# Kernel tuning notes

Hardware: AMD Instinct MI355X
Metric: run time of the kernel (lower is better)

## Reference

```python
import jax, jax.numpy as jnp
import numpy as np

B, H, L, TAU, THETA = 8192, 256, 4, 8, 8


def setup_inputs() -> dict:
    key = jax.random.key(0)
    ks = jax.random.split(key, 16)
    w = lambda k, shape: (jax.random.normal(k, shape, jnp.float32) * 0.02)
    return {
        "x": jax.random.normal(ks[0], (B, H), jnp.float32),
        "t_att": jax.random.normal(ks[1], (L, TAU, B, H), jnp.float32),
        "s_att": jax.random.normal(ks[2], (L, TAU, B, H), jnp.float32),
        "embed_w": w(ks[3], (H, H)),
        "embed_b": jnp.zeros((H,), jnp.float32),
        "wtn": w(ks[4], (L, H, H)),
        "btn": jnp.zeros((L, H), jnp.float32),
        "wsn": w(ks[5], (L, H, H)),
        "bsn": jnp.zeros((L, H), jnp.float32),
        "wt": w(ks[6], (L, 3 * H, H)),
        "bt": jnp.zeros((L, 3 * H), jnp.float32),
        "ws": w(ks[7], (L, 3 * H, H)),
        "bs": jnp.zeros((L, 3 * H), jnp.float32),
        "out_w": w(ks[8], (H, H)),
        "out_b": jnp.zeros((H,), jnp.float32),
    }


def _forward(x, t_att, s_att, embed_w, embed_b, wtn, btn, wsn, bsn, wt, bt, ws, bs, out_w, out_b):
    n_layers, tau = t_att.shape[0], t_att.shape[1]
    b, h = x.shape
    scale = 1.0 / np.sqrt(h).astype(np.float32)
    theta = THETA

    S = x @ embed_w.T + embed_b  # embed: [B, H]
    # rolling spatial buffers, start as theta zero entries
    t_sp = jnp.zeros((theta, b, h), x.dtype)
    s_sp = jnp.zeros((theta, b, h), x.dtype)

    for i in range(n_layers):
        T_last = t_att[i, -1]  # [B, H]
        # append current S_t / last T_t to spatial buffers, keep last theta
        s_sp = jnp.concatenate([s_sp[1:], S[None]], axis=0)
        t_sp = jnp.concatenate([t_sp[1:], T_last[None]], axis=0)
        # s_att[i].append(S_t); slice last tau -> keys include current S
        s_keys = jnp.concatenate([s_att[i, 1:], S[None]], axis=0)  # [tau, B, H]
        t_vals = t_att[i]  # [tau, B, H]

        s_next = S @ wsn[i].T + bsn[i]
        t_next = T_last @ wtn[i].T + btn[i]

        # temporal attention over last-tau history
        w_t = jax.nn.softmax(jnp.einsum('kbh,bh->kb', s_keys, s_next) * scale, axis=0)
        T_trend = jnp.einsum('kb,kbh->bh', w_t, t_vals)
        t_gate = jax.nn.sigmoid(t_next)
        T_fusion = T_last * t_gate + (1.0 - t_gate) * T_trend

        # spatial attention over last-theta buffer
        w_s = jax.nn.softmax(jnp.einsum('kbh,bh->kb', t_sp, t_next) * scale, axis=0)
        S_trend = jnp.einsum('kb,kbh->bh', w_s, s_sp)
        s_gate = jax.nn.sigmoid(s_next)
        S_fusion = S * s_gate + (1.0 - s_gate) * S_trend

        Tc = T_fusion @ wt[i].T + bt[i]  # [B, 3H]
        Sc = S_fusion @ ws[i].T + bs[i]
        t_g, t_t_, t_s_ = jnp.split(Tc, 3, axis=-1)
        s_g, s_t_, s_s_ = jnp.split(Sc, 3, axis=-1)
        Tg = jax.nn.sigmoid(t_g)
        Sg = jax.nn.sigmoid(s_g)
        # T_new feeds the (stateful) history; S carries to next layer
        S = Sg * s_s_ + (1.0 - Sg) * t_s_

    return jnp.tanh(S @ out_w.T + out_b)


def reference(x, t_att, s_att, embed_w, embed_b, wtn, btn, wsn, bsn, wt, bt, ws, bs, out_w, out_b):
    return _forward(x, t_att, s_att, embed_w, embed_b, wtn, btn, wsn, bsn, wt, bt, ws, bs, out_w, out_b)
```

## Files before the change

kernel.cpp:

```cpp
#include <hip/hip_runtime.h>
#include <cmath>

typedef __attribute__((ext_vector_type(8))) short short8;
typedef __attribute__((ext_vector_type(4))) float f32x4;
typedef __attribute__((ext_vector_type(4))) unsigned short us4;
typedef unsigned short u16;

#define BATCH 8192
#define HDIM  256
static constexpr size_t BH = (size_t)BATCH * HDIM;
#define LPAD 264

__device__ __forceinline__ u16 f2bf(float f) {
    union { float f; unsigned u; } v; v.f = f;
    unsigned r = v.u + 0x7FFFu + ((v.u >> 16) & 1u);
    return (u16)(r >> 16);
}
__device__ __forceinline__ float bf2f(u16 u) {
    union { unsigned u; float f; } v; v.u = ((unsigned)u) << 16;
    return v.f;
}
__device__ __forceinline__ float sigmoidf_(float x) {
    return 1.f / (1.f + __expf(-x));
}
__device__ __forceinline__ short8 cvt8(const float* p) {
    f32x4 lo = *(const f32x4*)p, hi = *(const f32x4*)(p + 4);
    short8 t;
    t[0] = (short)f2bf(lo[0]); t[1] = (short)f2bf(lo[1]);
    t[2] = (short)f2bf(lo[2]); t[3] = (short)f2bf(lo[3]);
    t[4] = (short)f2bf(hi[0]); t[5] = (short)f2bf(hi[1]);
    t[6] = (short)f2bf(hi[2]); t[7] = (short)f2bf(hi[3]);
    return t;
}
__device__ __forceinline__ float dot4(const f32x4& a, const float* b) {
    return a[0] * b[0] + a[1] * b[1] + a[2] * b[2] + a[3] * b[3];
}
template<int N>
__device__ __forceinline__ void vmwait() {
    asm volatile("s_waitcnt vmcnt(%0)" :: "n"(N) : "memory");
    __builtin_amdgcn_sched_barrier(0);
}

__global__ __launch_bounds__(256) void convert_weights(
    const float* __restrict__ embed_w, const float* __restrict__ wtn,
    const float* __restrict__ wsn, const float* __restrict__ wt,
    const float* __restrict__ ws, const float* __restrict__ out_w,
    u16* __restrict__ dst)
{
    int idx = blockIdx.x * 256 + threadIdx.x;
    int e = idx * 4;
    if (e >= 22 * 65536) return;
    int c = e >> 16, o = e & 65535;
    const float* src;
    if (c == 0)      src = embed_w + o;
    else if (c < 5)  src = wtn + (size_t)(c - 1) * 65536 + o;
    else if (c < 9)  src = wsn + (size_t)(c - 5) * 65536 + o;
    else if (c < 13) src = wt + (size_t)(c - 9) * 768 * 256 + 512 * 256 + o;
    else if (c < 17) src = ws + (size_t)(c - 13) * 768 * 256 + o;
    else if (c < 21) src = ws + (size_t)(c - 17) * 768 * 256 + 512 * 256 + o;
    else             src = out_w + o;
    f32x4 v = *(const f32x4*)src;
    us4 r;
#pragma unroll
    for (int j = 0; j < 4; ++j) r[j] = f2bf(v[j]);
    *(us4*)(dst + e) = r;
}

template<int I>
__device__ __forceinline__ void attn_row(
    const float* __restrict__ t_att, const float* __restrict__ s_att,
    const u16* __restrict__ S_hist,
    int brow, int rr, int lane,
    u16 (&sn_lds)[16][LPAD], u16 (&tn_lds)[16][LPAD],
    u16 (&tf_lds)[16][LPAD], u16 (&sf_lds)[16][LPAD])
{
    const float scale = 0.0625f;
    const size_t ro = (size_t)brow * 256 + lane * 4;
    const float* sa = s_att + (size_t)I * 8 * BH + ro;
    const float* ta = t_att + (size_t)I * 8 * BH + ro;

    us4 scu;
    us4 shu[I > 0 ? I : 1];
    asm volatile("global_load_dwordx2 %0, %1, off"
                 : "=v"(scu) : "v"(S_hist + (size_t)I * BH + ro));
#pragma unroll
    for (int jj = 0; jj < I; ++jj)
        asm volatile("global_load_dwordx2 %0, %1, off"
                     : "=v"(shu[jj]) : "v"(S_hist + (size_t)jj * BH + ro));

    f32x4 dbuf[8 + I];
#pragma unroll
    for (int kk = 0; kk < 7; ++kk)
        asm volatile("global_load_dwordx4 %0, %1, off"
                     : "=v"(dbuf[kk]) : "v"(sa + (size_t)(kk + 1) * BH));
#pragma unroll
    for (int jj = 0; jj < I; ++jj)
        asm volatile("global_load_dwordx4 %0, %1, off"
                     : "=v"(dbuf[7 + jj]) : "v"(t_att + ((size_t)jj * 8 + 7) * BH + ro));
    asm volatile("global_load_dwordx4 %0, %1, off"
                 : "=v"(dbuf[7 + I]) : "v"(ta + (size_t)7 * BH));

    f32x4 tbuf[7];
#pragma unroll
    for (int kk = 0; kk < 7; ++kk)
        asm volatile("global_load_dwordx4 %0, %1, off"
                     : "=v"(tbuf[kk]) : "v"(ta + (size_t)kk * BH));

    us4 snu = *(const us4*)&sn_lds[rr][lane * 4];
    us4 tnu = *(const us4*)&tn_lds[rr][lane * 4];
    float sn[4], tn[4];
#pragma unroll
    for (int j = 0; j < 4; ++j) { sn[j] = bf2f(snu[j]); tn[j] = bf2f(tnu[j]); }

    vmwait<7>();

    float Sc[4];
#pragma unroll
    for (int j = 0; j < 4; ++j) Sc[j] = bf2f(scu[j]);

    constexpr int NV = 9 + I;
    float v[NV];
#pragma unroll
    for (int kk = 0; kk < 7; ++kk) v[kk] = dot4(dbuf[kk], sn);
    v[7] = Sc[0] * sn[0] + Sc[1] * sn[1] + Sc[2] * sn[2] + Sc[3] * sn[3];
#pragma unroll
    for (int jj = 0; jj < I; ++jj) v[8 + jj] = dot4(dbuf[7 + jj], tn);
    v[8 + I] = dot4(dbuf[7 + I], tn);

#pragma unroll
    for (int o = 32; o > 0; o >>= 1)
#pragma unroll
        for (int u = 0; u < NV; ++u) v[u] += __shfl_xor(v[u], o);

    float m = v[0] * scale;
#pragma unroll
    for (int kk = 1; kk < 8; ++kk) m = fmaxf(m, v[kk] * scale);
    float w8[8], den = 0.f;
#pragma unroll
    for (int kk = 0; kk < 8; ++kk) { w8[kk] = __expf(v[kk] * scale - m); den += w8[kk]; }
    float inv = 1.f / den;

    vmwait<0>();

    float Tt[4];
#pragma unroll
    for (int j = 0; j < 4; ++j) Tt[j] = w8[7] * dbuf[7 + I][j];
#pragma unroll
    for (int kk = 0; kk < 7; ++kk)
#pragma unroll
        for (int j = 0; j < 4; ++j) Tt[j] += w8[kk] * tbuf[kk][j];
    us4 ot;
#pragma unroll
    for (int j = 0; j < 4; ++j) {
        float g = sigmoidf_(tn[j]);
        ot[j] = f2bf(dbuf[7 + I][j] * g + (1.f - g) * Tt[j] * inv);
    }
    *(us4*)&tf_lds[rr][lane * 4] = ot;

    float ms = fmaxf(0.f, v[8 + I] * scale);
#pragma unroll
    for (int jj = 0; jj < I; ++jj) ms = fmaxf(ms, v[8 + jj] * scale);
    float dens = (float)(7 - I) * __expf(-ms);
    float St[4];
    {
        float w = __expf(v[8 + I] * scale - ms);
        dens += w;
#pragma unroll
        for (int j = 0; j < 4; ++j) St[j] = w * Sc[j];
    }
#pragma unroll
    for (int jj = 0; jj < I; ++jj) {
        float w = __expf(v[8 + jj] * scale - ms);
        dens += w;
#pragma unroll
        for (int j = 0; j < 4; ++j) St[j] += w * bf2f(shu[jj][j]);
    }
    float invs = 1.f / dens;
    us4 os;
#pragma unroll
    for (int j = 0; j < 4; ++j) {
        float g = sigmoidf_(sn[j]);
        os[j] = f2bf(Sc[j] * g + (1.f - g) * St[j] * invs);
    }
    *(us4*)&sf_lds[rr][lane * 4] = os;
}

template<int I>
__device__ __forceinline__ void layer_body(
    const float* __restrict__ t_att, const float* __restrict__ s_att,
    u16* __restrict__ S_hist, const u16* __restrict__ Wbf,
    const float* __restrict__ btn, const float* __restrict__ bsn,
    const float* __restrict__ bt, const float* __restrict__ bs,
    u16 (&sn_lds)[16][LPAD], u16 (&tn_lds)[16][LPAD],
    u16 (&tf_lds)[16][LPAD], u16 (&sf_lds)[16][LPAD],
    int lane, int wave, int lr, int kg, int row0)
{
    {
        const int g = wave >> 1;
        const int n0 = (wave & 1) * 128;
        const u16* Wm = Wbf + (size_t)((g ? 1 : 5) + I) * 65536;
        const float* bias = (g ? btn : bsn) + I * 256;
        f32x4 acc[8] = {};
        for (int k0 = 0; k0 < 256; k0 += 32) {
            int k = k0 + kg * 8;
            short8 a;
            if (g == 0) a = *(const short8*)(S_hist + (size_t)I * BH + (size_t)(row0 + lr) * 256 + k);
            else        a = cvt8(t_att + ((size_t)I * 8 + 7) * BH + (size_t)(row0 + lr) * 256 + k);
#pragma unroll
            for (int nf = 0; nf < 8; ++nf) {
                short8 b = *(const short8*)(Wm + (size_t)(n0 + nf * 16 + lr) * 256 + k);
                acc[nf] = __builtin_amdgcn_mfma_f32_16x16x32_bf16(a, b, acc[nf], 0, 0, 0);
            }
        }
        u16 (*dst)[LPAD] = g ? tn_lds : sn_lds;
#pragma unroll
        for (int nf = 0; nf < 8; ++nf) {
            int n = n0 + nf * 16 + lr;
            float bn = bias[n];
#pragma unroll
            for (int r = 0; r < 4; ++r)
                dst[kg * 4 + r][n] = f2bf(acc[nf][r] + bn);
        }
    }
    __syncthreads();

#pragma unroll 1
    for (int q = 0; q < 4; ++q) {
        int rr = wave * 4 + q;
        attn_row<I>(t_att, s_att, S_hist, row0 + rr, rr, lane,
                    sn_lds, tn_lds, tf_lds, sf_lds);
    }
    __syncthreads();

    {
        const int n0 = wave * 64;
        const u16* Wt3 = Wbf + (size_t)(9  + I) * 65536;
        const u16* Ws1 = Wbf + (size_t)(13 + I) * 65536;
        const u16* Ws3 = Wbf + (size_t)(17 + I) * 65536;
        f32x4 aT[4] = {}, aG[4] = {}, aS[4] = {};
        for (int k0 = 0; k0 < 256; k0 += 32) {
            int k = k0 + kg * 8;
            short8 at = *(const short8*)(&tf_lds[lr][k]);
            short8 as = *(const short8*)(&sf_lds[lr][k]);
#pragma unroll
            for (int nf = 0; nf < 4; ++nf) {
                size_t wo = (size_t)(n0 + nf * 16 + lr) * 256 + k;
                aT[nf] = __builtin_amdgcn_mfma_f32_16x16x32_bf16(at, *(const short8*)(Wt3 + wo), aT[nf], 0, 0, 0);
                aG[nf] = __builtin_amdgcn_mfma_f32_16x16x32_bf16(as, *(const short8*)(Ws1 + wo), aG[nf], 0, 0, 0);
                aS[nf] = __builtin_amdgcn_mfma_f32_16x16x32_bf16(as, *(const short8*)(Ws3 + wo), aS[nf], 0, 0, 0);
            }
        }
        u16* Sout = S_hist + (size_t)(I + 1) * BH;
        const float* b1 = bt + I * 768 + 512;
        const float* b2 = bs + I * 768;
        const float* b3 = bs + I * 768 + 512;
#pragma unroll
        for (int nf = 0; nf < 4; ++nf) {
            int n = n0 + nf * 16 + lr;
            float bb1 = b1[n], bb2 = b2[n], bb3 = b3[n];
#pragma unroll
            for (int r = 0; r < 4; ++r) {
                float gv = sigmoidf_(aG[nf][r] + bb2);
                float vv = gv * (aS[nf][r] + bb3) + (1.f - gv) * (aT[nf][r] + bb1);
                Sout[(size_t)(row0 + kg * 4 + r) * 256 + n] = f2bf(vv);
            }
        }
    }
    __syncthreads();
}

__global__ __launch_bounds__(256, 2) void stau_mega(
    const float* __restrict__ x,
    const float* __restrict__ t_att, const float* __restrict__ s_att,
    u16* __restrict__ S_hist, const u16* __restrict__ Wbf,
    const float* __restrict__ embed_b,
    const float* __restrict__ btn, const float* __restrict__ bsn,
    const float* __restrict__ bt, const float* __restrict__ bs,
    const float* __restrict__ out_b,
    float* __restrict__ outp)
{
    __shared__ __align__(16) u16 sn_lds[16][LPAD];
    __shared__ __align__(16) u16 tn_lds[16][LPAD];
    __shared__ __align__(16) u16 tf_lds[16][LPAD];
    __shared__ __align__(16) u16 sf_lds[16][LPAD];

    const int lane = threadIdx.x & 63;
    const int wave = threadIdx.x >> 6;
    const int lr = lane & 15;
    const int kg = lane >> 4;
    const int row0 = blockIdx.x * 16;

    {
        const int n0 = wave * 64;
        f32x4 acc[4] = {};
        for (int k0 = 0; k0 < 256; k0 += 32) {
            int k = k0 + kg * 8;
            short8 a = cvt8(x + (size_t)(row0 + lr) * 256 + k);
#pragma unroll
            for (int nf = 0; nf < 4; ++nf) {
                short8 b = *(const short8*)(Wbf + (size_t)(n0 + nf * 16 + lr) * 256 + k);
                acc[nf] = __builtin_amdgcn_mfma_f32_16x16x32_bf16(a, b, acc[nf], 0, 0, 0);
            }
        }
#pragma unroll
        for (int nf = 0; nf < 4; ++nf) {
            int n = n0 + nf * 16 + lr;
            float bn = embed_b[n];
#pragma unroll
            for (int r = 0; r < 4; ++r)
                S_hist[(size_t)(row0 + kg * 4 + r) * 256 + n] = f2bf(acc[nf][r] + bn);
        }
    }
    __syncthreads();

    layer_body<0>(t_att, s_att, S_hist, Wbf, btn, bsn, bt, bs,
                  sn_lds, tn_lds, tf_lds, sf_lds, lane, wave, lr, kg, row0);
    layer_body<1>(t_att, s_att, S_hist, Wbf, btn, bsn, bt, bs,
                  sn_lds, tn_lds, tf_lds, sf_lds, lane, wave, lr, kg, row0);
    layer_body<2>(t_att, s_att, S_hist, Wbf, btn, bsn, bt, bs,
                  sn_lds, tn_lds, tf_lds, sf_lds, lane, wave, lr, kg, row0);
    layer_body<3>(t_att, s_att, S_hist, Wbf, btn, bsn, bt, bs,
                  sn_lds, tn_lds, tf_lds, sf_lds, lane, wave, lr, kg, row0);

    {
        const int n0 = wave * 64;
        const u16* Wo = Wbf + (size_t)21 * 65536;
        const u16* S4 = S_hist + (size_t)4 * BH;
        f32x4 acc[4] = {};
        for (int k0 = 0; k0 < 256; k0 += 32) {
            int k = k0 + kg * 8;
            short8 a = *(const short8*)(S4 + (size_t)(row0 + lr) * 256 + k);
#pragma unroll
            for (int nf = 0; nf < 4; ++nf) {
                short8 b = *(const short8*)(Wo + (size_t)(n0 + nf * 16 + lr) * 256 + k);
                acc[nf] = __builtin_amdgcn_mfma_f32_16x16x32_bf16(a, b, acc[nf], 0, 0, 0);
            }
        }
#pragma unroll
        for (int nf = 0; nf < 4; ++nf) {
            int n = n0 + nf * 16 + lr;
            float bn = out_b[n];
#pragma unroll
            for (int r = 0; r < 4; ++r)
                outp[(size_t)(row0 + kg * 4 + r) * 256 + n] = tanhf(acc[nf][r] + bn);
        }
    }
}

extern "C" void kernel_launch(void* const* d_in, const int* in_sizes, int n_in,
                              void* d_out, int out_size, void* d_ws, size_t ws_size,
                              hipStream_t stream)
{
    (void)in_sizes; (void)n_in; (void)out_size; (void)ws_size;
    const float* x       = (const float*)d_in[0];
    const float* t_att   = (const float*)d_in[1];
    const float* s_att   = (const float*)d_in[2];
    const float* embed_w = (const float*)d_in[3];
    const float* embed_b = (const float*)d_in[4];
    const float* wtn     = (const float*)d_in[5];
    const float* btn     = (const float*)d_in[6];
    const float* wsn     = (const float*)d_in[7];
    const float* bsn     = (const float*)d_in[8];
    const float* wt      = (const float*)d_in[9];
    const float* bt      = (const float*)d_in[10];
    const float* ws_in   = (const float*)d_in[11];
    const float* bs      = (const float*)d_in[12];
    const float* out_w   = (const float*)d_in[13];
    const float* out_b   = (const float*)d_in[14];

    u16* wsp    = (u16*)d_ws;
    u16* Wbf    = wsp;
    u16* S_hist = wsp + (size_t)22 * 65536;

    convert_weights<<<1408, 256, 0, stream>>>(embed_w, wtn, wsn, wt, ws_in, out_w, Wbf);

    stau_mega<<<BATCH / 16, 256, 0, stream>>>(
        x, t_att, s_att, S_hist, Wbf, embed_b, btn, bsn, bt, bs, out_b, (float*)d_out);
}
```

Measured before the change: 312.8 us.

## Warp-specialize mega kernel with async global-to-LDS staging of attention history

Restructures the fused kernel into 512-thread blocks of 4 rows, with 4 producer waves and 4 consumer waves. Producer waves stream the per-layer t_att/s_att history straight into double-buffered LDS slabs using global_load_lds, prefetching two layers ahead, and also compute the attention rows. Consumer waves run the MFMA projections. Each block now uses only 4 of the 16 MFMA rows, so most matrix work is padding. Weight reads per row also rise fourfold, and the large LDS footprint limits occupancy, in exchange for hiding the HBM latency of the history tensors.

Result: slower. 881.7 us (+181.9%).

```diff
diff --git a/kernel.cpp b/kernel.cpp
--- a/kernel.cpp
+++ b/kernel.cpp
@@ -1,5 +1,6 @@
 #include <hip/hip_runtime.h>
 #include <cmath>
+#include <type_traits>
 
 typedef __attribute__((ext_vector_type(8))) short short8;
 typedef __attribute__((ext_vector_type(4))) float f32x4;
@@ -7,9 +8,7 @@
 typedef unsigned short u16;
 
 #define BATCH 8192
-#define HDIM  256
-static constexpr size_t BH = (size_t)BATCH * HDIM;
-#define LPAD 264
+static constexpr size_t BH = (size_t)BATCH * 256;
 
 __device__ __forceinline__ u16 f2bf(float f) {
     union { float f; unsigned u; } v; v.f = f;
@@ -39,6 +38,18 @@
 __device__ __forceinline__ void vmwait() {
     asm volatile("s_waitcnt vmcnt(%0)" :: "n"(N) : "memory");
     __builtin_amdgcn_sched_barrier(0);
+}
+__device__ __forceinline__ void lgkm0() {
+    asm volatile("s_waitcnt lgkmcnt(0)" ::: "memory");
+    __builtin_amdgcn_sched_barrier(0);
+}
+__device__ __forceinline__ void bar() { __builtin_amdgcn_s_barrier(); }
+
+__device__ __forceinline__ void gl_lds16(const float* g, float* l) {
+    __builtin_amdgcn_global_load_lds(
+        (const __attribute__((address_space(1))) unsigned int*)(const void*)g,
+        (__attribute__((address_space(3))) unsigned int*)(void*)l,
+        16, 0, 0);
 }
 
 __global__ __launch_bounds__(256) void convert_weights(
@@ -66,66 +77,60 @@
     *(us4*)(dst + e) = r;
 }
 
+template<int J>
+__device__ __forceinline__ void stage_row(float* buf,
+    const float* __restrict__ t_att, const float* __restrict__ s_att,
+    int row0, int r, int lane)
+{
+    constexpr int NS = (J & 1) ? 18 : 17;
+    const size_t ro = (size_t)(row0 + r) * 256 + lane * 4;
+    float* base = buf + (size_t)r * NS * 256;
+#pragma unroll
+    for (int kk = 0; kk < 7; ++kk)
+        gl_lds16(s_att + ((size_t)J * 8 + 1 + kk) * BH + ro, base + kk * 256);
+#pragma unroll
+    for (int kk = 0; kk < 8; ++kk)
+        gl_lds16(t_att + ((size_t)J * 8 + kk) * BH + ro, base + (7 + kk) * 256);
+#pragma unroll
+    for (int jj = 0; jj < J; ++jj)
+        gl_lds16(t_att + ((size_t)jj * 8 + 7) * BH + ro, base + (15 + jj) * 256);
+}
+
+struct LState {
+    float slabA[4][17][256];
+    float slabB[4][18][256];
+    u16 snl[4][264];
+    u16 tnl[4][264];
+    u16 tfl[4][264];
+    u16 sfl[4][264];
+    u16 scsh[4][4][256];
+};
+
 template<int I>
-__device__ __forceinline__ void attn_row(
-    const float* __restrict__ t_att, const float* __restrict__ s_att,
-    const u16* __restrict__ S_hist,
-    int brow, int rr, int lane,
-    u16 (&sn_lds)[16][LPAD], u16 (&tn_lds)[16][LPAD],
-    u16 (&tf_lds)[16][LPAD], u16 (&sf_lds)[16][LPAD])
-{
+__device__ __forceinline__ void attn_row_lds(const float* cur, int r, int lane, LState& L)
+{
+    constexpr int NS = (I & 1) ? 18 : 17;
     const float scale = 0.0625f;
-    const size_t ro = (size_t)brow * 256 + lane * 4;
-    const float* sa = s_att + (size_t)I * 8 * BH + ro;
-    const float* ta = t_att + (size_t)I * 8 * BH + ro;
-
-    us4 scu;
-    us4 shu[I > 0 ? I : 1];
-    asm volatile("global_load_dwordx2 %0, %1, off"
-                 : "=v"(scu) : "v"(S_hist + (size_t)I * BH + ro));
-#pragma unroll
-    for (int jj = 0; jj < I; ++jj)
-        asm volatile("global_load_dwordx2 %0, %1, off"
-                     : "=v"(shu[jj]) : "v"(S_hist + (size_t)jj * BH + ro));
-
-    f32x4 dbuf[8 + I];
-#pragma unroll
-    for (int kk = 0; kk < 7; ++kk)
-        asm volatile("global_load_dwordx4 %0, %1, off"
-                     : "=v"(dbuf[kk]) : "v"(sa + (size_t)(kk + 1) * BH));
-#pragma unroll
-    for (int jj = 0; jj < I; ++jj)
-        asm volatile("global_load_dwordx4 %0, %1, off"
-                     : "=v"(dbuf[7 + jj]) : "v"(t_att + ((size_t)jj * 8 + 7) * BH + ro));
-    asm volatile("global_load_dwordx4 %0, %1, off"
-                 : "=v"(dbuf[7 + I]) : "v"(ta + (size_t)7 * BH));
-
-    f32x4 tbuf[7];
-#pragma unroll
-    for (int kk = 0; kk < 7; ++kk)
-        asm volatile("global_load_dwordx4 %0, %1, off"
-                     : "=v"(tbuf[kk]) : "v"(ta + (size_t)kk * BH));
-
-    us4 snu = *(const us4*)&sn_lds[rr][lane * 4];
-    us4 tnu = *(const us4*)&tn_lds[rr][lane * 4];
-    float sn[4], tn[4];
-#pragma unroll
-    for (int j = 0; j < 4; ++j) { sn[j] = bf2f(snu[j]); tn[j] = bf2f(tnu[j]); }
-
-    vmwait<7>();
-
-    float Sc[4];
-#pragma unroll
-    for (int j = 0; j < 4; ++j) Sc[j] = bf2f(scu[j]);
+    const float* rowp = cur + (size_t)r * NS * 256;
+
+    us4 snu = *(const us4*)&L.snl[r][lane * 4];
+    us4 tnu = *(const us4*)&L.tnl[r][lane * 4];
+    us4 scu = *(const us4*)&L.scsh[r][0][lane * 4];
+    float sn[4], tn[4], Sc[4];
+#pragma unroll
+    for (int j = 0; j < 4; ++j) { sn[j] = bf2f(snu[j]); tn[j] = bf2f(tnu[j]); Sc[j] = bf2f(scu[j]); }
 
     constexpr int NV = 9 + I;
     float v[NV];
 #pragma unroll
-    for (int kk = 0; kk < 7; ++kk) v[kk] = dot4(dbuf[kk], sn);
+    for (int kk = 0; kk < 7; ++kk)
+        v[kk] = dot4(*(const f32x4*)(rowp + kk * 256 + lane * 4), sn);
     v[7] = Sc[0] * sn[0] + Sc[1] * sn[1] + Sc[2] * sn[2] + Sc[3] * sn[3];
 #pragma unroll
-    for (int jj = 0; jj < I; ++jj) v[8 + jj] = dot4(dbuf[7 + jj], tn);
-    v[8 + I] = dot4(dbuf[7 + I], tn);
+    for (int jj = 0; jj < I; ++jj)
+        v[8 + jj] = dot4(*(const f32x4*)(rowp + (15 + jj) * 256 + lane * 4), tn);
+    f32x4 tav7 = *(const f32x4*)(rowp + 14 * 256 + lane * 4);
+    v[8 + I] = dot4(tav7, tn);
 
 #pragma unroll
     for (int o = 32; o > 0; o >>= 1)
@@ -140,22 +145,20 @@
     for (int kk = 0; kk < 8; ++kk) { w8[kk] = __expf(v[kk] * scale - m); den += w8[kk]; }
     float inv = 1.f / den;
 
-    vmwait<0>();
-
-    float Tt[4];
-#pragma unroll
-    for (int j = 0; j < 4; ++j) Tt[j] = w8[7] * dbuf[7 + I][j];
-#pragma unroll
-    for (int kk = 0; kk < 7; ++kk)
-#pragma unroll
-        for (int j = 0; j < 4; ++j) Tt[j] += w8[kk] * tbuf[kk][j];
+    float Tt[4] = {0.f, 0.f, 0.f, 0.f};
+#pragma unroll
+    for (int kk = 0; kk < 8; ++kk) {
+        f32x4 tv = *(const f32x4*)(rowp + (7 + kk) * 256 + lane * 4);
+#pragma unroll
+        for (int j = 0; j < 4; ++j) Tt[j] += w8[kk] * tv[j];
+    }
     us4 ot;
 #pragma unroll
     for (int j = 0; j < 4; ++j) {
         float g = sigmoidf_(tn[j]);
-        ot[j] = f2bf(dbuf[7 + I][j] * g + (1.f - g) * Tt[j] * inv);
-    }
-    *(us4*)&tf_lds[rr][lane * 4] = ot;
+        ot[j] = f2bf(tav7[j] * g + (1.f - g) * Tt[j] * inv);
+    }
+    *(us4*)&L.tfl[r][lane * 4] = ot;
 
     float ms = fmaxf(0.f, v[8 + I] * scale);
 #pragma unroll
@@ -172,8 +175,9 @@
     for (int jj = 0; jj < I; ++jj) {
         float w = __expf(v[8 + jj] * scale - ms);
         dens += w;
-#pragma unroll
-        for (int j = 0; j < 4; ++j) St[j] += w * bf2f(shu[jj][j]);
+        us4 shu = *(const us4*)&L.scsh[r][1 + jj][lane * 4];
+#pragma unroll
+        for (int j = 0; j < 4; ++j) St[j] += w * bf2f(shu[j]);
     }
     float invs = 1.f / dens;
     us4 os;
@@ -182,7 +186,7 @@
         float g = sigmoidf_(sn[j]);
         os[j] = f2bf(Sc[j] * g + (1.f - g) * St[j] * invs);
     }
-    *(us4*)&sf_lds[rr][lane * 4] = os;
+    *(us4*)&L.sfl[r][lane * 4] = os;
 }
 
 template<int I>
@@ -191,57 +195,69 @@
     u16* __restrict__ S_hist, const u16* __restrict__ Wbf,
     const float* __restrict__ btn, const float* __restrict__ bsn,
     const float* __restrict__ bt, const float* __restrict__ bs,
-    u16 (&sn_lds)[16][LPAD], u16 (&tn_lds)[16][LPAD],
-    u16 (&tf_lds)[16][LPAD], u16 (&sf_lds)[16][LPAD],
-    int lane, int wave, int lr, int kg, int row0)
-{
-    {
-        const int g = wave >> 1;
-        const int n0 = (wave & 1) * 128;
-        const u16* Wm = Wbf + (size_t)((g ? 1 : 5) + I) * 65536;
-        const float* bias = (g ? btn : bsn) + I * 256;
-        f32x4 acc[8] = {};
+    LState& L, int lane, int wave, int lr, int kg, int row0, bool prod, int pr, int n0)
+{
+    constexpr int NS = (I & 1) ? 18 : 17;
+    float* cur = (I & 1) ? &L.slabB[0][0][0] : &L.slabA[0][0][0];
+
+    if (!prod) {
+        const int cw = wave;
+        const size_t ro = (size_t)(row0 + cw) * 256 + lane * 4;
+        *(us4*)&L.scsh[cw][0][lane * 4] = *(const us4*)(S_hist + (size_t)I * BH + ro);
+#pragma unroll
+        for (int jj = 0; jj < I; ++jj)
+            *(us4*)&L.scsh[cw][1 + jj][lane * 4] = *(const us4*)(S_hist + (size_t)jj * BH + ro);
+
+        const u16* Wsn = Wbf + (size_t)(5 + I) * 65536;
+        const u16* Wtn = Wbf + (size_t)(1 + I) * 65536;
+        const u16* Arow = S_hist + (size_t)I * BH + (size_t)(row0 + (lr < 4 ? lr : 0)) * 256;
+        const float* Trow = cur + (size_t)(lr < 4 ? lr : 0) * NS * 256 + 14 * 256;
+        f32x4 accS[4] = {}, accT[4] = {};
         for (int k0 = 0; k0 < 256; k0 += 32) {
             int k = k0 + kg * 8;
-            short8 a;
-            if (g == 0) a = *(const short8*)(S_hist + (size_t)I * BH + (size_t)(row0 + lr) * 256 + k);
-            else        a = cvt8(t_att + ((size_t)I * 8 + 7) * BH + (size_t)(row0 + lr) * 256 + k);
-#pragma unroll
-            for (int nf = 0; nf < 8; ++nf) {
-                short8 b = *(const short8*)(Wm + (size_t)(n0 + nf * 16 + lr) * 256 + k);
-                acc[nf] = __builtin_amdgcn_mfma_f32_16x16x32_bf16(a, b, acc[nf], 0, 0, 0);
-            }
-        }
-        u16 (*dst)[LPAD] = g ? tn_lds : sn_lds;
-#pragma unroll
-        for (int nf = 0; nf < 8; ++nf) {
-            int n = n0 + nf * 16 + lr;
-            float bn = bias[n];
-#pragma unroll
-            for (int r = 0; r < 4; ++r)
-                dst[kg * 4 + r][n] = f2bf(acc[nf][r] + bn);
-        }
-    }
-    __syncthreads();
-
-#pragma unroll 1
-    for (int q = 0; q < 4; ++q) {
-        int rr = wave * 4 + q;
-        attn_row<I>(t_att, s_att, S_hist, row0 + rr, rr, lane,
-                    sn_lds, tn_lds, tf_lds, sf_lds);
-    }
-    __syncthreads();
-
-    {
-        const int n0 = wave * 64;
-        const u16* Wt3 = Wbf + (size_t)(9  + I) * 65536;
+            short8 aS = *(const short8*)(Arow + k);
+            short8 aT = cvt8(Trow + k);
+#pragma unroll
+            for (int nf = 0; nf < 4; ++nf) {
+                size_t wo = (size_t)(n0 + nf * 16 + lr) * 256 + k;
+                accS[nf] = __builtin_amdgcn_mfma_f32_16x16x32_bf16(aS, *(const short8*)(Wsn + wo), accS[nf], 0, 0, 0);
+                accT[nf] = __builtin_amdgcn_mfma_f32_16x16x32_bf16(aT, *(const short8*)(Wtn + wo), accT[nf], 0, 0, 0);
+            }
+        }
+        if (kg == 0) {
+#pragma unroll
+            for (int nf = 0; nf < 4; ++nf) {
+                int n = n0 + nf * 16 + lr;
+                float bS = bsn[I * 256 + n], bT = btn[I * 256 + n];
+#pragma unroll
+                for (int r = 0; r < 4; ++r) {
+                    L.snl[r][n] = f2bf(accS[nf][r] + bS);
+                    L.tnl[r][n] = f2bf(accT[nf][r] + bT);
+                }
+            }
+        }
+        lgkm0();
+    }
+    bar();
+
+    if (prod) {
+        attn_row_lds<I>(cur, pr, lane, L);
+        lgkm0();
+        if constexpr (I + 2 <= 3)
+            stage_row<I + 2>(cur, t_att, s_att, row0, pr, lane);
+    }
+    bar();
+
+    if (!prod) {
+        const u16* Wt3 = Wbf + (size_t)(9 + I) * 65536;
         const u16* Ws1 = Wbf + (size_t)(13 + I) * 65536;
         const u16* Ws3 = Wbf + (size_t)(17 + I) * 65536;
+        const int ar = (lr < 4 ? lr : 0);
         f32x4 aT[4] = {}, aG[4] = {}, aS[4] = {};
         for (int k0 = 0; k0 < 256; k0 += 32) {
             int k = k0 + kg * 8;
-            short8 at = *(const short8*)(&tf_lds[lr][k]);
-            short8 as = *(const short8*)(&sf_lds[lr][k]);
+            short8 at = *(const short8*)(&L.tfl[ar][k]);
+            short8 as = *(const short8*)(&L.sfl[ar][k]);
 #pragma unroll
             for (int nf = 0; nf < 4; ++nf) {
                 size_t wo = (size_t)(n0 + nf * 16 + lr) * 256 + k;
@@ -250,26 +266,32 @@
                 aS[nf] = __builtin_amdgcn_mfma_f32_16x16x32_bf16(as, *(const short8*)(Ws3 + wo), aS[nf], 0, 0, 0);
             }
         }
-        u16* Sout = S_hist + (size_t)(I + 1) * BH;
-        const float* b1 = bt + I * 768 + 512;
-        const float* b2 = bs + I * 768;
-        const float* b3 = bs + I * 768 + 512;
-#pragma unroll
-        for (int nf = 0; nf < 4; ++nf) {
-            int n = n0 + nf * 16 + lr;
-            float bb1 = b1[n], bb2 = b2[n], bb3 = b3[n];
-#pragma unroll
-            for (int r = 0; r < 4; ++r) {
-                float gv = sigmoidf_(aG[nf][r] + bb2);
-                float vv = gv * (aS[nf][r] + bb3) + (1.f - gv) * (aT[nf][r] + bb1);
-                Sout[(size_t)(row0 + kg * 4 + r) * 256 + n] = f2bf(vv);
-            }
-        }
-    }
-    __syncthreads();
-}
-
-__global__ __launch_bounds__(256, 2) void stau_mega(
+        if (kg == 0) {
+            const float* b1 = bt + I * 768 + 512;
+            const float* b2 = bs + I * 768;
+            const float* b3 = bs + I * 768 + 512;
+#pragma unroll
+            for (int nf = 0; nf < 4; ++nf) {
+                int n = n0 + nf * 16 + lr;
+                float bb1 = b1[n], bb2 = b2[n], bb3 = b3[n];
+#pragma unroll
+                for (int r = 0; r < 4; ++r) {
+                    float gv = sigmoidf_(aG[nf][r] + bb2);
+                    float vv = gv * (aS[nf][r] + bb3) + (1.f - gv) * (aT[nf][r] + bb1);
+                    S_hist[(size_t)(I + 1) * BH + (size_t)(row0 + r) * 256 + n] = f2bf(vv);
+                }
+            }
+        }
+        vmwait<0>();
+    } else {
+        if constexpr (I == 0) vmwait<17>();
+        else if constexpr (I == 1) vmwait<18>();
+        else if constexpr (I == 2) vmwait<0>();
+    }
+    bar();
+}
+
+__global__ __launch_bounds__(512, 2) void stau_mega(
     const float* __restrict__ x,
     const float* __restrict__ t_att, const float* __restrict__ s_att,
     u16* __restrict__ S_hist, const u16* __restrict__ Wbf,
@@ -279,70 +301,74 @@
     const float* __restrict__ out_b,
     float* __restrict__ outp)
 {
-    __shared__ __align__(16) u16 sn_lds[16][LPAD];
-    __shared__ __align__(16) u16 tn_lds[16][LPAD];
-    __shared__ __align__(16) u16 tf_lds[16][LPAD];
-    __shared__ __align__(16) u16 sf_lds[16][LPAD];
+    __shared__ __align__(16) LState L;
 
     const int lane = threadIdx.x & 63;
     const int wave = threadIdx.x >> 6;
     const int lr = lane & 15;
     const int kg = lane >> 4;
-    const int row0 = blockIdx.x * 16;
-
-    {
-        const int n0 = wave * 64;
+    const int row0 = blockIdx.x * 4;
+    const bool prod = wave >= 4;
+    const int pr = wave - 4;
+    const int n0 = (wave & 3) * 64;
+
+    if (prod) {
+        stage_row<0>(&L.slabA[0][0][0], t_att, s_att, row0, pr, lane);
+        stage_row<1>(&L.slabB[0][0][0], t_att, s_att, row0, pr, lane);
+        vmwait<16>();
+    } else {
+        const float* Ax = x + (size_t)(row0 + (lr < 4 ? lr : 0)) * 256;
         f32x4 acc[4] = {};
         for (int k0 = 0; k0 < 256; k0 += 32) {
             int k = k0 + kg * 8;
-            short8 a = cvt8(x + (size_t)(row0 + lr) * 256 + k);
+            short8 a = cvt8(Ax + k);
 #pragma unroll
             for (int nf = 0; nf < 4; ++nf) {
                 short8 b = *(const short8*)(Wbf + (size_t)(n0 + nf * 16 + lr) * 256 + k);
                 acc[nf] = __builtin_amdgcn_mfma_f32_16x16x32_bf16(a, b, acc[nf], 0, 0, 0);
             }
         }
-#pragma unroll
-        for (int nf = 0; nf < 4; ++nf) {
-            int n = n0 + nf * 16 + lr;
-            float bn = embed_b[n];
-#pragma unroll
-            for (int r = 0; r < 4; ++r)
-                S_hist[(size_t)(row0 + kg * 4 + r) * 256 + n] = f2bf(acc[nf][r] + bn);
-        }
-    }
-    __syncthreads();
-
-    layer_body<0>(t_att, s_att, S_hist, Wbf, btn, bsn, bt, bs,
-                  sn_lds, tn_lds, tf_lds, sf_lds, lane, wave, lr, kg, row0);
-    layer_body<1>(t_att, s_att, S_hist, Wbf, btn, bsn, bt, bs,
-                  sn_lds, tn_lds, tf_lds, sf_lds, lane, wave, lr, kg, row0);
-    layer_body<2>(t_att, s_att, S_hist, Wbf, btn, bsn, bt, bs,
-                  sn_lds, tn_lds, tf_lds, sf_lds, lane, wave, lr, kg, row0);
-    layer_body<3>(t_att, s_att, S_hist, Wbf, btn, bsn, bt, bs,
-                  sn_lds, tn_lds, tf_lds, sf_lds, lane, wave, lr, kg, row0);
-
-    {
-        const int n0 = wave * 64;
+        if (kg == 0) {
+#pragma unroll
+            for (int nf = 0; nf < 4; ++nf) {
+                int n = n0 + nf * 16 + lr;
+                float bn = embed_b[n];
+#pragma unroll
+                for (int r = 0; r < 4; ++r)
+                    S_hist[(size_t)(row0 + r) * 256 + n] = f2bf(acc[nf][r] + bn);
+            }
+        }
+        vmwait<0>();
+    }
+    bar();
+
+    layer_body<0>(t_att, s_att, S_hist, Wbf, btn, bsn, bt, bs, L, lane, wave, lr, kg, row0, prod, pr, n0);
+    layer_body<1>(t_att, s_att, S_hist, Wbf, btn, bsn, bt, bs, L, lane, wave, lr, kg, row0, prod, pr, n0);
+    layer_body<2>(t_att, s_att, S_hist, Wbf, btn, bsn, bt, bs, L, lane, wave, lr, kg, row0, prod, pr, n0);
+    layer_body<3>(t_att, s_att, S_hist, Wbf, btn, bsn, bt, bs, L, lane, wave, lr, kg, row0, prod, pr, n0);
+
+    if (!prod) {
         const u16* Wo = Wbf + (size_t)21 * 65536;
-        const u16* S4 = S_hist + (size_t)4 * BH;
+        const u16* A4 = S_hist + (size_t)4 * BH + (size_t)(row0 + (lr < 4 ? lr : 0)) * 256;
         f32x4 acc[4] = {};
         for (int k0 = 0; k0 < 256; k0 += 32) {
             int k = k0 + kg * 8;
-            short8 a = *(const short8*)(S4 + (size_t)(row0 + lr) * 256 + k);
+            short8 a = *(const short8*)(A4 + k);
 #pragma unroll
             for (int nf = 0; nf < 4; ++nf) {
                 short8 b = *(const short8*)(Wo + (size_t)(n0 + nf * 16 + lr) * 256 + k);
                 acc[nf] = __builtin_amdgcn_mfma_f32_16x16x32_bf16(a, b, acc[nf], 0, 0, 0);
             }
         }
-#pragma unroll
-        for (int nf = 0; nf < 4; ++nf) {
-            int n = n0 + nf * 16 + lr;
-            float bn = out_b[n];
-#pragma unroll
-            for (int r = 0; r < 4; ++r)
-                outp[(size_t)(row0 + kg * 4 + r) * 256 + n] = tanhf(acc[nf][r] + bn);
+        if (kg == 0) {
+#pragma unroll
+            for (int nf = 0; nf < 4; ++nf) {
+                int n = n0 + nf * 16 + lr;
+                float bn = out_b[n];
+#pragma unroll
+                for (int r = 0; r < 4; ++r)
+                    outp[(size_t)(row0 + r) * 256 + n] = tanhf(acc[nf][r] + bn);
+            }
         }
     }
 }
@@ -374,6 +400,6 @@
 
     convert_weights<<<1408, 256, 0, stream>>>(embed_w, wtn, wsn, wt, ws_in, out_w, Wbf);
 
-    stau_mega<<<BATCH / 16, 256, 0, stream>>>(
+    stau_mega<<<BATCH / 4, 512, 0, stream>>>(
         x, t_att, s_att, S_hist, Wbf, embed_b, btn, bsn, bt, bs, out_b, (float*)d_out);
 }
```
